# Kernel optimization log

Measured on AMD Instinct MI355X. Metric: run time of the kernel, lower is better.

## Reference

```python
import jax, jax.numpy as jnp
import numpy as np

H = 1024
NH = 16
HD = H // NH
EPS = 1e-5


def setup_inputs() -> dict:
    key = jax.random.key(0)
    ks = jax.random.split(key, 16)
    B, LQ, LK = 2, 1024, 2048
    s = 1.0 / np.sqrt(H)
    inp = {
        "query": jax.random.normal(ks[0], (B, LQ, H), jnp.float32),
        "key": jax.random.normal(ks[1], (B, LK, H), jnp.float32),
        "value": jax.random.normal(ks[2], (B, LK, H), jnp.float32),
        "mask": jax.random.randint(ks[3], (B, LQ, LK), 0, 2, jnp.int32),
        "Wq": jax.random.normal(ks[4], (H, H), jnp.float32) * s,
        "bq": jnp.zeros((H,), jnp.float32),
        "Wk": jax.random.normal(ks[5], (H, H), jnp.float32) * s,
        "bk": jnp.zeros((H,), jnp.float32),
        "Wv": jax.random.normal(ks[6], (H, H), jnp.float32) * s,
        "bv": jnp.zeros((H,), jnp.float32),
        "Wo": jax.random.normal(ks[7], (H, H), jnp.float32) * s,
        "bo": jnp.zeros((H,), jnp.float32),
        "ln_g": jnp.ones((H,), jnp.float32),
        "ln_b": jnp.zeros((H,), jnp.float32),
    }
    return inp


def _split_heads(x, B, L):
    # [B, L, H] -> [B, NH, L, HD]
    return x.reshape(B, L, NH, HD).transpose(0, 2, 1, 3)


def reference(query, key, value, mask, Wq, bq, Wk, bk, Wv, bv, Wo, bo, ln_g, ln_b):
    B, LQ, _ = query.shape
    LK = key.shape[1]
    # projections (torch Linear: x @ W.T + b)
    Q = _split_heads(query @ Wq.T + bq, B, LQ)   # [B,NH,LQ,HD]
    K = _split_heads(key   @ Wk.T + bk, B, LK)   # [B,NH,LK,HD]
    V = _split_heads(value @ Wv.T + bv, B, LK)   # [B,NH,LK,HD]
    scores = jnp.einsum('bhqd,bhkd->bhqk', Q, K) / np.sqrt(HD)
    scores = jnp.where(mask[:, None, :, :] == 0, jnp.float32(-1e9), scores)
    attn = jax.nn.softmax(scores, axis=-1)
    # dropout is identity in eval mode
    ctx = jnp.einsum('bhqk,bhkd->bhqd', attn, V)            # [B,NH,LQ,HD]
    ctx = ctx.transpose(0, 2, 1, 3).reshape(B, LQ, H)       # [B,LQ,H]
    out = ctx @ Wo.T + bo
    x = out + query
    mu = jnp.mean(x, axis=-1, keepdims=True)
    var = jnp.mean(jnp.square(x - mu), axis=-1, keepdims=True)
    return (x - mu) / jnp.sqrt(var + EPS) * ln_g + ln_b
```

## Files before the change

### kernel.cpp

```cpp
#include <hip/hip_runtime.h>
#include <hip/hip_bf16.h>

typedef __hip_bfloat16 hbf16;

#define Hdim 1024
#define NHEAD 16
#define HDIM 64
#define BATCH 2
#define LQ 1024
#define LK 2048
#define LN_EPS 1e-5f

typedef __bf16 bfv8 __attribute__((ext_vector_type(8)));
typedef float floatx4 __attribute__((ext_vector_type(4)));
typedef union { bfv8 v; __bf16 b[8]; unsigned short s[8]; } bfu8;

#define BK 32
#define LDS_PITCH 40
#define QT 64
#define KT 64
#define KS_PITCH 72
#define VT_OFF(d) ((d) * 72 + (((d) >> 3) << 3))
#define PS_OFF(r) ((r) * 72 + (((r) >> 2) << 3))

__device__ inline bfv8 cvt2(const float4 x, const float4 y) {
    bfv8 r = {(__bf16)x.x, (__bf16)x.y, (__bf16)x.z, (__bf16)x.w,
              (__bf16)y.x, (__bf16)y.y, (__bf16)y.z, (__bf16)y.w};
    return r;
}

__global__ __launch_bounds__(256) void proj3_mfma(
    const float* __restrict__ q_in, const float* __restrict__ k_in,
    const float* __restrict__ v_in,
    const float* __restrict__ Wq, const float* __restrict__ bq,
    const float* __restrict__ Wk, const float* __restrict__ bk,
    const float* __restrict__ Wv, const float* __restrict__ bv,
    hbf16* __restrict__ Qp, hbf16* __restrict__ Kp, hbf16* __restrict__ Vp) {
    const int z = blockIdx.z;
    if (z == 0 && blockIdx.y >= (BATCH * LQ) / 64) return;
    const float* A; const float* W; const float* bias; hbf16* out; float scale;
    if (z == 0)      { A = q_in; W = Wq; bias = bq; out = Qp; scale = 0.125f; }
    else if (z == 1) { A = k_in; W = Wk; bias = bk; out = Kp; scale = 1.0f; }
    else             { A = v_in; W = Wv; bias = bv; out = Vp; scale = 1.0f; }

    __shared__ __align__(16) __bf16 As[64 * LDS_PITCH];
    __shared__ __align__(16) __bf16 Bs[64 * LDS_PITCH];
    const int tid = threadIdx.x;
    const int lane = tid & 63;
    const int w = tid >> 6;
    const int wm = w & 1, wn = w >> 1;
    const int rowBase = blockIdx.y * 64;
    const int colBase = blockIdx.x * 64;
    const int sr = tid >> 2;
    const int scg = (tid & 3) * 8;
    const int lr = lane & 15;
    const int quad = lane >> 4;

    floatx4 acc[2][2] = {};

    for (int k0 = 0; k0 < Hdim; k0 += BK) {
        const float* ap = A + (size_t)(rowBase + sr) * Hdim + k0 + scg;
        bfv8 av = cvt2(((const float4*)ap)[0], ((const float4*)ap)[1]);
        const float* wp = W + (size_t)(colBase + sr) * Hdim + k0 + scg;
        bfv8 bv8 = cvt2(((const float4*)wp)[0], ((const float4*)wp)[1]);
        __syncthreads();
        *(bfv8*)&As[sr * LDS_PITCH + scg] = av;
        *(bfv8*)&Bs[sr * LDS_PITCH + scg] = bv8;
        __syncthreads();

        bfv8 bf[2];
#pragma unroll
        for (int nt = 0; nt < 2; ++nt)
            bf[nt] = *(const bfv8*)&Bs[(wn * 32 + nt * 16 + lr) * LDS_PITCH + quad * 8];
#pragma unroll
        for (int mt = 0; mt < 2; ++mt) {
            bfv8 af = *(const bfv8*)&As[(wm * 32 + mt * 16 + lr) * LDS_PITCH + quad * 8];
#pragma unroll
            for (int nt = 0; nt < 2; ++nt)
                acc[mt][nt] = __builtin_amdgcn_mfma_f32_16x16x32_bf16(af, bf[nt], acc[mt][nt], 0, 0, 0);
        }
    }

#pragma unroll
    for (int mt = 0; mt < 2; ++mt)
#pragma unroll
        for (int nt = 0; nt < 2; ++nt) {
            const int n = colBase + wn * 32 + nt * 16 + lr;
            const float bn = bias[n];
#pragma unroll
            for (int rr = 0; rr < 4; ++rr) {
                const int m = rowBase + wm * 32 + mt * 16 + quad * 4 + rr;
                out[(size_t)m * Hdim + n] = __float2bfloat16((acc[mt][nt][rr] + bn) * scale);
            }
        }
}

__global__ __launch_bounds__(256) void gemm_mfma_f32(const float* __restrict__ A,
                                                     const float* __restrict__ W,
                                                     const float* __restrict__ bias,
                                                     hbf16* __restrict__ out,
                                                     float scale) {
    __shared__ __align__(16) __bf16 As[64 * LDS_PITCH];
    __shared__ __align__(16) __bf16 Bs[64 * LDS_PITCH];
    const int tid = threadIdx.x;
    const int lane = tid & 63;
    const int w = tid >> 6;
    const int wm = w & 1, wn = w >> 1;
    const int rowBase = blockIdx.y * 64;
    const int colBase = blockIdx.x * 64;
    const int sr = tid >> 2;
    const int scg = (tid & 3) * 8;
    const int lr = lane & 15;
    const int quad = lane >> 4;

    floatx4 acc[2][2] = {};

    for (int k0 = 0; k0 < Hdim; k0 += BK) {
        const float* ap = A + (size_t)(rowBase + sr) * Hdim + k0 + scg;
        bfv8 av = cvt2(((const float4*)ap)[0], ((const float4*)ap)[1]);
        const float* wp = W + (size_t)(colBase + sr) * Hdim + k0 + scg;
        bfv8 bv = cvt2(((const float4*)wp)[0], ((const float4*)wp)[1]);
        __syncthreads();
        *(bfv8*)&As[sr * LDS_PITCH + scg] = av;
        *(bfv8*)&Bs[sr * LDS_PITCH + scg] = bv;
        __syncthreads();

        bfv8 bf[2];
#pragma unroll
        for (int nt = 0; nt < 2; ++nt)
            bf[nt] = *(const bfv8*)&Bs[(wn * 32 + nt * 16 + lr) * LDS_PITCH + quad * 8];
#pragma unroll
        for (int mt = 0; mt < 2; ++mt) {
            bfv8 af = *(const bfv8*)&As[(wm * 32 + mt * 16 + lr) * LDS_PITCH + quad * 8];
#pragma unroll
            for (int nt = 0; nt < 2; ++nt)
                acc[mt][nt] = __builtin_amdgcn_mfma_f32_16x16x32_bf16(af, bf[nt], acc[mt][nt], 0, 0, 0);
        }
    }

#pragma unroll
    for (int mt = 0; mt < 2; ++mt)
#pragma unroll
        for (int nt = 0; nt < 2; ++nt) {
            const int n = colBase + wn * 32 + nt * 16 + lr;
            const float bn = bias[n];
#pragma unroll
            for (int rr = 0; rr < 4; ++rr) {
                const int m = rowBase + wm * 32 + mt * 16 + quad * 4 + rr;
                out[(size_t)m * Hdim + n] = __float2bfloat16((acc[mt][nt][rr] + bn) * scale);
            }
        }
}

__global__ __launch_bounds__(256) void gemm_mfma_ctx(const hbf16* __restrict__ A,
                                                     const float* __restrict__ W,
                                                     const float* __restrict__ bias,
                                                     const float* __restrict__ resid,
                                                     float* __restrict__ out) {
    __shared__ __align__(16) __bf16 As[64 * LDS_PITCH];
    __shared__ __align__(16) __bf16 Bs[64 * LDS_PITCH];
    const int tid = threadIdx.x;
    const int lane = tid & 63;
    const int w = tid >> 6;
    const int wm = w & 1, wn = w >> 1;
    const int rowBase = blockIdx.y * 64;
    const int colBase = blockIdx.x * 64;
    const int sr = tid >> 2;
    const int scg = (tid & 3) * 8;
    const int lr = lane & 15;
    const int quad = lane >> 4;

    floatx4 acc[2][2] = {};

    for (int k0 = 0; k0 < Hdim; k0 += BK) {
        bfv8 av = *(const bfv8*)(A + (size_t)(rowBase + sr) * Hdim + k0 + scg);
        const float* wp = W + (size_t)(colBase + sr) * Hdim + k0 + scg;
        bfv8 bv = cvt2(((const float4*)wp)[0], ((const float4*)wp)[1]);
        __syncthreads();
        *(bfv8*)&As[sr * LDS_PITCH + scg] = av;
        *(bfv8*)&Bs[sr * LDS_PITCH + scg] = bv;
        __syncthreads();

        bfv8 bf[2];
#pragma unroll
        for (int nt = 0; nt < 2; ++nt)
            bf[nt] = *(const bfv8*)&Bs[(wn * 32 + nt * 16 + lr) * LDS_PITCH + quad * 8];
#pragma unroll
        for (int mt = 0; mt < 2; ++mt) {
            bfv8 af = *(const bfv8*)&As[(wm * 32 + mt * 16 + lr) * LDS_PITCH + quad * 8];
#pragma unroll
            for (int nt = 0; nt < 2; ++nt)
                acc[mt][nt] = __builtin_amdgcn_mfma_f32_16x16x32_bf16(af, bf[nt], acc[mt][nt], 0, 0, 0);
        }
    }

#pragma unroll
    for (int mt = 0; mt < 2; ++mt)
#pragma unroll
        for (int nt = 0; nt < 2; ++nt) {
            const int n = colBase + wn * 32 + nt * 16 + lr;
            const float bn = bias[n];
#pragma unroll
            for (int rr = 0; rr < 4; ++rr) {
                const int m = rowBase + wm * 32 + mt * 16 + quad * 4 + rr;
                out[(size_t)m * Hdim + n] = acc[mt][nt][rr] + bn + resid[(size_t)m * Hdim + n];
            }
        }
}

__global__ __launch_bounds__(256) void mask_prep_st(const int* __restrict__ mask,
                                                    hbf16* __restrict__ mbias) {
    const int t = blockIdx.x;
    const int kt = t & 31;
    const int qb = (t >> 5) & 15;
    const int b = t >> 9;
    const int tid = threadIdx.x;
    const int w = tid >> 6;
    const int lane = tid & 63;
    const int quad = lane >> 4;
    const int u = lane & 15;
    const int qrow = qb * 64 + w * 16 + quad * 4;
    const int kcol = kt * 64 + u;
    const int* mp = mask + ((size_t)(b * LQ + qrow)) * LK + kcol;

    bfu8 v0, v1;
#pragma unroll
    for (int ns = 0; ns < 4; ++ns)
#pragma unroll
        for (int rr = 0; rr < 4; ++rr) {
            const int mv = mp[(size_t)rr * LK + ns * 16];
            const __bf16 bias = (mv == 0) ? (__bf16)(-1e9f) : (__bf16)(-10.0f);
            const int j = ns * 4 + rr;
            if (j < 8) v0.b[j] = bias; else v1.b[j - 8] = bias;
        }
    __bf16* dst = (__bf16*)mbias + (size_t)t * 4096 + tid * 16;
    *(bfv8*)dst = v0.v;
    *(bfv8*)(dst + 8) = v1.v;
}

__global__ __launch_bounds__(256, 4) void attn_split(const hbf16* __restrict__ Qp,
                                                     const hbf16* __restrict__ Kp,
                                                     const hbf16* __restrict__ Vp,
                                                     const hbf16* __restrict__ mbias,
                                                     float* __restrict__ Opart,
                                                     float* __restrict__ lpart) {
    const int qb = blockIdx.x;
    const int h = blockIdx.y;
    const int b = blockIdx.z >> 1;
    const int sp = blockIdx.z & 1;
    const int tid = threadIdx.x;
    const int lane = tid & 63;
    const int w = tid >> 6;
    const int u = lane & 15;
    const int quad = lane >> 4;
    const int qBase = qb * QT;

    __shared__ __align__(16) __bf16 Ks[64 * KS_PITCH];
    __shared__ __align__(16) __bf16 Vt[4672];
    __shared__ __align__(16) __bf16 Ps[4][1184];

    const int qrow_frag = qBase + w * 16 + u;
    const hbf16* qptr = Qp + (size_t)(b * LQ + qrow_frag) * Hdim + h * HDIM + quad * 8;
    const bfv8 af_q0 = *(const bfv8*)qptr;
    const bfv8 af_q1 = *(const bfv8*)(qptr + 32);

    float l_acc[4] = {0.f, 0.f, 0.f, 0.f};
    floatx4 acc_o[4];
#pragma unroll
    for (int nd = 0; nd < 4; ++nd) acc_o[nd] = (floatx4){0.f, 0.f, 0.f, 0.f};

    const int sk = tid >> 2;
    const int sdg = (tid & 3) * 16;
    const int vk2 = (tid >> 3) * 2;
    const int vd0 = (tid & 7) * 8;
    const __bf16* mbT = (const __bf16*)mbias + (size_t)(b * 16 + qb) * 32 * 4096 + tid * 16;

    const int kt0 = sp * (LK / KT / 2);
    for (int kt = kt0; kt < kt0 + (LK / KT / 2); ++kt) {
        const int kBase = kt * KT;

        bfu8 mb0, mb1;
        mb0.v = *(const bfv8*)(mbT + (size_t)kt * 4096);
        mb1.v = *(const bfv8*)(mbT + (size_t)kt * 4096 + 8);

        const hbf16* vp0 = Vp + (size_t)(b * LK + kBase + vk2) * Hdim + h * HDIM + vd0;
        bfu8 v0, v1;
        v0.v = *(const bfv8*)vp0;
        v1.v = *(const bfv8*)(vp0 + Hdim);
        const hbf16* kp = Kp + (size_t)(b * LK + kBase + sk) * Hdim + h * HDIM + sdg;
        const bfv8 kv0 = *(const bfv8*)kp;
        const bfv8 kv1 = *(const bfv8*)(kp + 8);

        __syncthreads();
        *(bfv8*)&Ks[sk * KS_PITCH + sdg] = kv0;
        *(bfv8*)&Ks[sk * KS_PITCH + sdg + 8] = kv1;
#pragma unroll
        for (int i = 0; i < 8; ++i) {
            unsigned int pk = (unsigned int)v0.s[i] | ((unsigned int)v1.s[i] << 16);
            *(unsigned int*)&Vt[VT_OFF(vd0 + i) + vk2] = pk;
        }
        __syncthreads();

        floatx4 acc_s[4];
#pragma unroll
        for (int ns = 0; ns < 4; ++ns) {
            const bfv8 bk0 = *(const bfv8*)&Ks[(ns * 16 + u) * KS_PITCH + quad * 8];
            const bfv8 bk1 = *(const bfv8*)&Ks[(ns * 16 + u) * KS_PITCH + quad * 8 + 32];
            floatx4 a = (floatx4){0.f, 0.f, 0.f, 0.f};
            a = __builtin_amdgcn_mfma_f32_16x16x32_bf16(af_q0, bk0, a, 0, 0, 0);
            a = __builtin_amdgcn_mfma_f32_16x16x32_bf16(af_q1, bk1, a, 0, 0, 0);
            acc_s[ns] = a;
        }

        __bf16* Pw = Ps[w];
#pragma unroll
        for (int ns = 0; ns < 4; ++ns)
#pragma unroll
            for (int rr = 0; rr < 4; ++rr) {
                const int j = ns * 4 + rr;
                const float bias = (j < 8) ? (float)mb0.b[j] : (float)mb1.b[j - 8];
                const float p = __expf(acc_s[ns][rr] + bias);
                Pw[PS_OFF(quad * 4 + rr) + ns * 16 + u] = (__bf16)p;
                l_acc[rr] += p;
            }

        const bfv8 af_p0 = *(const bfv8*)&Pw[PS_OFF(u) + quad * 8];
        const bfv8 af_p1 = *(const bfv8*)&Pw[PS_OFF(u) + quad * 8 + 32];
#pragma unroll
        for (int nd = 0; nd < 4; ++nd) {
            const bfv8 bv0 = *(const bfv8*)&Vt[VT_OFF(nd * 16 + u) + quad * 8];
            const bfv8 bv1 = *(const bfv8*)&Vt[VT_OFF(nd * 16 + u) + quad * 8 + 32];
            acc_o[nd] = __builtin_amdgcn_mfma_f32_16x16x32_bf16(af_p0, bv0, acc_o[nd], 0, 0, 0);
            acc_o[nd] = __builtin_amdgcn_mfma_f32_16x16x32_bf16(af_p1, bv1, acc_o[nd], 0, 0, 0);
        }
    }

#pragma unroll
    for (int rr = 0; rr < 4; ++rr) {
        float l = l_acc[rr];
        l += __shfl_xor(l, 1, 64);
        l += __shfl_xor(l, 2, 64);
        l += __shfl_xor(l, 4, 64);
        l += __shfl_xor(l, 8, 64);
        const int qrow = qBase + w * 16 + quad * 4 + rr;
        const size_t m = (size_t)(b * LQ + qrow);
        float* orow = Opart + (size_t)sp * (BATCH * LQ * Hdim) + m * Hdim + h * HDIM;
#pragma unroll
        for (int nd = 0; nd < 4; ++nd)
            orow[nd * 16 + u] = acc_o[nd][rr];
        if (u == 0)
            lpart[(size_t)sp * (BATCH * LQ * NHEAD) + m * NHEAD + h] = l;
    }
}

__global__ __launch_bounds__(256) void merge_ctx(const float* __restrict__ Opart,
                                                 const float* __restrict__ lpart,
                                                 hbf16* __restrict__ ctx) {
    const size_t m = blockIdx.x;
    const int t = threadIdx.x;
    const int kk = t * 4;
    const int h = kk >> 6;
    const float l = lpart[m * NHEAD + h] +
                    lpart[(size_t)(BATCH * LQ * NHEAD) + m * NHEAD + h];
    const float invl = 1.0f / l;
    const float4 a = ((const float4*)(Opart + m * Hdim))[t];
    const float4 c = ((const float4*)(Opart + (size_t)(BATCH * LQ * Hdim) + m * Hdim))[t];
    hbf16* crow = ctx + m * Hdim + kk;
    crow[0] = __float2bfloat16((a.x + c.x) * invl);
    crow[1] = __float2bfloat16((a.y + c.y) * invl);
    crow[2] = __float2bfloat16((a.z + c.z) * invl);
    crow[3] = __float2bfloat16((a.w + c.w) * invl);
}

__global__ __launch_bounds__(256, 4) void attn_flash_st(const hbf16* __restrict__ Qp,
                                                        const hbf16* __restrict__ Kp,
                                                        const hbf16* __restrict__ Vp,
                                                        const hbf16* __restrict__ mbias,
                                                        hbf16* __restrict__ ctx) {
    const int qb = blockIdx.x;
    const int h = blockIdx.y;
    const int b = blockIdx.z;
    const int tid = threadIdx.x;
    const int lane = tid & 63;
    const int w = tid >> 6;
    const int u = lane & 15;
    const int quad = lane >> 4;
    const int qBase = qb * QT;

    __shared__ __align__(16) __bf16 Ks[64 * KS_PITCH];
    __shared__ __align__(16) __bf16 Vt[4672];
    __shared__ __align__(16) __bf16 Ps[4][1184];

    const int qrow_frag = qBase + w * 16 + u;
    const hbf16* qptr = Qp + (size_t)(b * LQ + qrow_frag) * Hdim + h * HDIM + quad * 8;
    const bfv8 af_q0 = *(const bfv8*)qptr;
    const bfv8 af_q1 = *(const bfv8*)(qptr + 32);

    float l_acc[4] = {0.f, 0.f, 0.f, 0.f};
    floatx4 acc_o[4];
#pragma unroll
    for (int nd = 0; nd < 4; ++nd) acc_o[nd] = (floatx4){0.f, 0.f, 0.f, 0.f};

    const int sk = tid >> 2;
    const int sdg = (tid & 3) * 16;
    const int vk2 = (tid >> 3) * 2;
    const int vd0 = (tid & 7) * 8;
    const __bf16* mbT = (const __bf16*)mbias + (size_t)(b * 16 + qb) * 32 * 4096 + tid * 16;

    for (int kt = 0; kt < LK / KT; ++kt) {
        const int kBase = kt * KT;

        bfu8 mb0, mb1;
        mb0.v = *(const bfv8*)(mbT + (size_t)kt * 4096);
        mb1.v = *(const bfv8*)(mbT + (size_t)kt * 4096 + 8);

        const hbf16* vp0 = Vp + (size_t)(b * LK + kBase + vk2) * Hdim + h * HDIM + vd0;
        bfu8 v0, v1;
        v0.v = *(const bfv8*)vp0;
        v1.v = *(const bfv8*)(vp0 + Hdim);
        const hbf16* kp = Kp + (size_t)(b * LK + kBase + sk) * Hdim + h * HDIM + sdg;
        const bfv8 kv0 = *(const bfv8*)kp;
        const bfv8 kv1 = *(const bfv8*)(kp + 8);

        __syncthreads();
        *(bfv8*)&Ks[sk * KS_PITCH + sdg] = kv0;
        *(bfv8*)&Ks[sk * KS_PITCH + sdg + 8] = kv1;
#pragma unroll
        for (int i = 0; i < 8; ++i) {
            unsigned int pk = (unsigned int)v0.s[i] | ((unsigned int)v1.s[i] << 16);
            *(unsigned int*)&Vt[VT_OFF(vd0 + i) + vk2] = pk;
        }
        __syncthreads();

        floatx4 acc_s[4];
#pragma unroll
        for (int ns = 0; ns < 4; ++ns) {
            const bfv8 bk0 = *(const bfv8*)&Ks[(ns * 16 + u) * KS_PITCH + quad * 8];
            const bfv8 bk1 = *(const bfv8*)&Ks[(ns * 16 + u) * KS_PITCH + quad * 8 + 32];
            floatx4 a = (floatx4){0.f, 0.f, 0.f, 0.f};
            a = __builtin_amdgcn_mfma_f32_16x16x32_bf16(af_q0, bk0, a, 0, 0, 0);
            a = __builtin_amdgcn_mfma_f32_16x16x32_bf16(af_q1, bk1, a, 0, 0, 0);
            acc_s[ns] = a;
        }

        __bf16* Pw = Ps[w];
#pragma unroll
        for (int ns = 0; ns < 4; ++ns)
#pragma unroll
            for (int rr = 0; rr < 4; ++rr) {
                const int j = ns * 4 + rr;
                const float bias = (j < 8) ? (float)mb0.b[j] : (float)mb1.b[j - 8];
                const float p = __expf(acc_s[ns][rr] + bias);
                Pw[PS_OFF(quad * 4 + rr) + ns * 16 + u] = (__bf16)p;
                l_acc[rr] += p;
            }

        const bfv8 af_p0 = *(const bfv8*)&Pw[PS_OFF(u) + quad * 8];
        const bfv8 af_p1 = *(const bfv8*)&Pw[PS_OFF(u) + quad * 8 + 32];
#pragma unroll
        for (int nd = 0; nd < 4; ++nd) {
            const bfv8 bv0 = *(const bfv8*)&Vt[VT_OFF(nd * 16 + u) + quad * 8];
            const bfv8 bv1 = *(const bfv8*)&Vt[VT_OFF(nd * 16 + u) + quad * 8 + 32];
            acc_o[nd] = __builtin_amdgcn_mfma_f32_16x16x32_bf16(af_p0, bv0, acc_o[nd], 0, 0, 0);
            acc_o[nd] = __builtin_amdgcn_mfma_f32_16x16x32_bf16(af_p1, bv1, acc_o[nd], 0, 0, 0);
        }
    }

#pragma unroll
    for (int rr = 0; rr < 4; ++rr) {
        float l = l_acc[rr];
        l += __shfl_xor(l, 1, 64);
        l += __shfl_xor(l, 2, 64);
        l += __shfl_xor(l, 4, 64);
        l += __shfl_xor(l, 8, 64);
        const float invl = 1.0f / l;
        const int qrow = qBase + w * 16 + quad * 4 + rr;
        hbf16* crow = ctx + (size_t)(b * LQ + qrow) * Hdim + h * HDIM;
#pragma unroll
        for (int nd = 0; nd < 4; ++nd)
            crow[nd * 16 + u] = __float2bfloat16(acc_o[nd][rr] * invl);
    }
}

__global__ __launch_bounds__(256) void ln_kernel(float* __restrict__ x,
                                                 const float* __restrict__ g,
                                                 const float* __restrict__ beta) {
    const int row = blockIdx.x;
    float* xr = x + (size_t)row * Hdim;
    __shared__ float red[256];
    const int tid = threadIdx.x;

    const float4 xi = ((const float4*)xr)[tid];
    red[tid] = xi.x + xi.y + xi.z + xi.w;
    __syncthreads();
    for (int st = 128; st > 0; st >>= 1) {
        if (tid < st) red[tid] += red[tid + st];
        __syncthreads();
    }
    const float mu = red[0] * (1.0f / Hdim);
    __syncthreads();
    {
        float dx = xi.x - mu, dy = xi.y - mu, dz = xi.z - mu, dw = xi.w - mu;
        red[tid] = dx * dx + dy * dy + dz * dz + dw * dw;
    }
    __syncthreads();
    for (int st = 128; st > 0; st >>= 1) {
        if (tid < st) red[tid] += red[tid + st];
        __syncthreads();
    }
    const float rstd = rsqrtf(red[0] * (1.0f / Hdim) + LN_EPS);

    const float4 g4 = ((const float4*)g)[tid];
    const float4 b4 = ((const float4*)beta)[tid];
    float4 y;
    y.x = (xi.x - mu) * rstd * g4.x + b4.x;
    y.y = (xi.y - mu) * rstd * g4.y + b4.y;
    y.z = (xi.z - mu) * rstd * g4.z + b4.z;
    y.w = (xi.w - mu) * rstd * g4.w + b4.w;
    ((float4*)xr)[tid] = y;
}

__device__ inline float wave_red_sum(float v) {
    v += __shfl_down(v, 32, 64);
    v += __shfl_down(v, 16, 64);
    v += __shfl_down(v, 8, 64);
    v += __shfl_down(v, 4, 64);
    v += __shfl_down(v, 2, 64);
    v += __shfl_down(v, 1, 64);
    return v;
}

__global__ __launch_bounds__(256) void fused_mha(
    const float* __restrict__ q_in, const float* __restrict__ k_in,
    const float* __restrict__ v_in, const int* __restrict__ mask,
    const float* __restrict__ Wq, const float* __restrict__ bq,
    const float* __restrict__ Wk, const float* __restrict__ bk,
    const float* __restrict__ Wv, const float* __restrict__ bv,
    const float* __restrict__ Wo, const float* __restrict__ bo,
    const float* __restrict__ ln_g, const float* __restrict__ ln_b,
    float* __restrict__ out) {
    const int q = blockIdx.x;
    const int b = blockIdx.y;
    const int tid = threadIdx.x;
    const int lane = tid & 63;
    const int w = tid >> 6;

    __shared__ float qrow[Hdim];
    __shared__ float qt[Hdim];
    __shared__ float sc[LK];
    __shared__ float u[Hdim];
    __shared__ float ctxv[Hdim];
    __shared__ float Qh[HDIM];
    __shared__ float red[256];
    __shared__ float sb_sh;

    const float* qp = q_in + (size_t)(b * LQ + q) * Hdim;
    for (int i = tid; i < Hdim; i += 256) qrow[i] = qp[i];
    __syncthreads();

    const float* keyb = k_in + (size_t)b * LK * Hdim;
    const float* valb = v_in + (size_t)b * LK * Hdim;
    const int* mrow = mask + (size_t)(b * LQ + q) * LK;

    for (int h = 0; h < NHEAD; ++h) {
        for (int dd = w; dd < HDIM; dd += 4) {
            const float4* wrow = (const float4*)(Wq + (size_t)(h * HDIM + dd) * Hdim);
            const float4* q4 = (const float4*)qrow;
            float p = 0.f;
#pragma unroll
            for (int i0 = 0; i0 < 4; ++i0) {
                float4 a = wrow[i0 * 64 + lane];
                float4 c = q4[i0 * 64 + lane];
                p += a.x * c.x + a.y * c.y + a.z * c.z + a.w * c.w;
            }
            p = wave_red_sum(p);
            if (lane == 0) Qh[dd] = p + bq[h * HDIM + dd];
        }
        __syncthreads();

        if (tid < HDIM) red[tid] = Qh[tid] * bk[h * HDIM + tid];

        float4 s4 = {0.f, 0.f, 0.f, 0.f};
        for (int d = 0; d < HDIM; ++d) {
            float4 a = ((const float4*)(Wk + (size_t)(h * HDIM + d) * Hdim))[tid];
            float qd = Qh[d];
            s4.x += a.x * qd;
            s4.y += a.y * qd;
            s4.z += a.z * qd;
            s4.w += a.w * qd;
        }
        __syncthreads();
        if (tid == 0) {
            float s = 0.f;
            for (int i = 0; i < HDIM; ++i) s += red[i];
            sb_sh = s;
        }
        ((float4*)qt)[tid] = s4;
        __syncthreads();
        const float sb = sb_sh;

        for (int k = w; k < LK; k += 4) {
            const float4* krow = (const float4*)(keyb + (size_t)k * Hdim);
            const float4* q4 = (const float4*)qt;
            float p = 0.f;
#pragma unroll
            for (int i0 = 0; i0 < 4; ++i0) {
                float4 a = krow[i0 * 64 + lane];
                float4 c = q4[i0 * 64 + lane];
                p += a.x * c.x + a.y * c.y + a.z * c.z + a.w * c.w;
            }
            p = wave_red_sum(p);
            if (lane == 0) {
                float s = (p + sb) * 0.125f;
                if (mrow[k] == 0) s = -1e9f;
                sc[k] = s;
            }
        }
        __syncthreads();

        float m = -1e30f;
        for (int k = tid; k < LK; k += 256) m = fmaxf(m, sc[k]);
        red[tid] = m;
        __syncthreads();
        for (int s = 128; s > 0; s >>= 1) {
            if (tid < s) red[tid] = fmaxf(red[tid], red[tid + s]);
            __syncthreads();
        }
        const float mx = red[0];
        __syncthreads();
        float sum = 0.f;
        for (int k = tid; k < LK; k += 256) {
            float e = __expf(sc[k] - mx);
            sc[k] = e;
            sum += e;
        }
        red[tid] = sum;
        __syncthreads();
        for (int s = 128; s > 0; s >>= 1) {
            if (tid < s) red[tid] += red[tid + s];
            __syncthreads();
        }
        const float inv = 1.0f / red[0];
        for (int k = tid; k < LK; k += 256) sc[k] *= inv;
        __syncthreads();

        {
            float4 acc = {0.f, 0.f, 0.f, 0.f};
            const float4* vb4 = (const float4*)valb;
#pragma unroll 4
            for (int k = 0; k < LK; ++k) {
                float p = sc[k];
                float4 a = vb4[(size_t)k * (Hdim / 4) + tid];
                acc.x += a.x * p;
                acc.y += a.y * p;
                acc.z += a.z * p;
                acc.w += a.w * p;
            }
            ((float4*)u)[tid] = acc;
        }
        __syncthreads();

        for (int dd = w; dd < HDIM; dd += 4) {
            const float4* wrow = (const float4*)(Wv + (size_t)(h * HDIM + dd) * Hdim);
            const float4* u4 = (const float4*)u;
            float p = 0.f;
#pragma unroll
            for (int i0 = 0; i0 < 4; ++i0) {
                float4 a = wrow[i0 * 64 + lane];
                float4 c = u4[i0 * 64 + lane];
                p += a.x * c.x + a.y * c.y + a.z * c.z + a.w * c.w;
            }
            p = wave_red_sum(p);
            if (lane == 0) ctxv[h * HDIM + dd] = p + bv[h * HDIM + dd];
        }
        __syncthreads();
    }

    for (int n = w; n < Hdim; n += 4) {
        const float4* wrow = (const float4*)(Wo + (size_t)n * Hdim);
        const float4* c4 = (const float4*)ctxv;
        float p = 0.f;
#pragma unroll
        for (int i0 = 0; i0 < 4; ++i0) {
            float4 a = wrow[i0 * 64 + lane];
            float4 c = c4[i0 * 64 + lane];
            p += a.x * c.x + a.y * c.y + a.z * c.z + a.w * c.w;
        }
        p = wave_red_sum(p);
        if (lane == 0) qt[n] = p + bo[n] + qrow[n];
    }
    __syncthreads();

    {
        const float4 x4 = ((const float4*)qt)[tid];
        red[tid] = x4.x + x4.y + x4.z + x4.w;
    }
    __syncthreads();
    for (int s = 128; s > 0; s >>= 1) {
        if (tid < s) red[tid] += red[tid + s];
        __syncthreads();
    }
    const float mu = red[0] * (1.0f / Hdim);
    __syncthreads();
    {
        const float4 x4 = ((const float4*)qt)[tid];
        float dx = x4.x - mu, dy = x4.y - mu, dz = x4.z - mu, dw = x4.w - mu;
        red[tid] = dx * dx + dy * dy + dz * dz + dw * dw;
    }
    __syncthreads();
    for (int s = 128; s > 0; s >>= 1) {
        if (tid < s) red[tid] += red[tid + s];
        __syncthreads();
    }
    const float rstd = rsqrtf(red[0] * (1.0f / Hdim) + LN_EPS);

    float* orow = out + (size_t)(b * LQ + q) * Hdim;
    const float4 x4 = ((const float4*)qt)[tid];
    const float4 g4 = ((const float4*)ln_g)[tid];
    const float4 b4 = ((const float4*)ln_b)[tid];
    float4 y;
    y.x = (x4.x - mu) * rstd * g4.x + b4.x;
    y.y = (x4.y - mu) * rstd * g4.y + b4.y;
    y.z = (x4.z - mu) * rstd * g4.z + b4.z;
    y.w = (x4.w - mu) * rstd * g4.w + b4.w;
    ((float4*)orow)[tid] = y;
}

extern "C" void kernel_launch(void* const* d_in, const int* in_sizes, int n_in,
                              void* d_out, int out_size, void* d_ws, size_t ws_size,
                              hipStream_t stream) {
    const float* query = (const float*)d_in[0];
    const float* key   = (const float*)d_in[1];
    const float* value = (const float*)d_in[2];
    const int*   mask  = (const int*)d_in[3];
    const float* Wq = (const float*)d_in[4];
    const float* bq = (const float*)d_in[5];
    const float* Wk = (const float*)d_in[6];
    const float* bk = (const float*)d_in[7];
    const float* Wv = (const float*)d_in[8];
    const float* bv = (const float*)d_in[9];
    const float* Wo = (const float*)d_in[10];
    const float* bo = (const float*)d_in[11];
    const float* ln_g = (const float*)d_in[12];
    const float* ln_b = (const float*)d_in[13];
    float* out = (float*)d_out;

    const size_t MB = 1024 * 1024;
    dim3 blk(256);

    if (ws_size >= 50 * MB) {
        char* p = (char*)d_ws;
        hbf16* Qp = (hbf16*)p;    p += 4 * MB;
        hbf16* Kp = (hbf16*)p;    p += 8 * MB;
        hbf16* Vp = (hbf16*)p;    p += 8 * MB;
        hbf16* ctxb = (hbf16*)p;  p += 4 * MB;
        hbf16* mbias = (hbf16*)p; p += 8 * MB;
        float* Opart = (float*)p; p += 16 * MB;
        float* lpart = (float*)p; p += 1 * MB;

        proj3_mfma<<<dim3(Hdim / 64, (BATCH * LK) / 64, 3), blk, 0, stream>>>(
            query, key, value, Wq, bq, Wk, bk, Wv, bv, Qp, Kp, Vp);
        mask_prep_st<<<dim3(1024), blk, 0, stream>>>(mask, mbias);

        attn_split<<<dim3(LQ / QT, NHEAD, BATCH * 2), blk, 0, stream>>>(
            Qp, Kp, Vp, mbias, Opart, lpart);
        merge_ctx<<<dim3(BATCH * LQ), blk, 0, stream>>>(Opart, lpart, ctxb);

        gemm_mfma_ctx<<<dim3(Hdim / 64, (BATCH * LQ) / 64), blk, 0, stream>>>(ctxb, Wo, bo, query, out);
        ln_kernel<<<BATCH * LQ, blk, 0, stream>>>(out, ln_g, ln_b);
    } else if (ws_size >= 32 * MB) {
        char* p = (char*)d_ws;
        hbf16* Qp = (hbf16*)p;    p += 4 * MB;
        hbf16* Kp = (hbf16*)p;    p += 8 * MB;
        hbf16* Vp = (hbf16*)p;    p += 8 * MB;
        hbf16* ctxb = (hbf16*)p;  p += 4 * MB;
        hbf16* mbias = (hbf16*)p; p += 8 * MB;

        gemm_mfma_f32<<<dim3(Hdim / 64, (BATCH * LQ) / 64), blk, 0, stream>>>(query, Wq, bq, Qp, 0.125f);
        gemm_mfma_f32<<<dim3(Hdim / 64, (BATCH * LK) / 64), blk, 0, stream>>>(key, Wk, bk, Kp, 1.0f);
        gemm_mfma_f32<<<dim3(Hdim / 64, (BATCH * LK) / 64), blk, 0, stream>>>(value, Wv, bv, Vp, 1.0f);
        mask_prep_st<<<dim3(1024), blk, 0, stream>>>(mask, mbias);
        attn_flash_st<<<dim3(LQ / QT, NHEAD, BATCH), blk, 0, stream>>>(Qp, Kp, Vp, mbias, ctxb);
        gemm_mfma_ctx<<<dim3(Hdim / 64, (BATCH * LQ) / 64), blk, 0, stream>>>(ctxb, Wo, bo, query, out);
        ln_kernel<<<BATCH * LQ, blk, 0, stream>>>(out, ln_g, ln_b);
    } else {
        fused_mha<<<dim3(LQ, BATCH), dim3(256), 0, stream>>>(
            query, key, value, mask, Wq, bq, Wk, bk, Wv, bv, Wo, bo, ln_g, ln_b, out);
    }
}
```

Baseline: 277.6 us.

## Pre-convert inputs to bf16 and use direct-to-LDS loads with 128x128 GEMM tiles

```diff
diff --git a/kernel.cpp b/kernel.cpp
--- a/kernel.cpp
+++ b/kernel.cpp
@@ -27,6 +27,177 @@
     bfv8 r = {(__bf16)x.x, (__bf16)x.y, (__bf16)x.z, (__bf16)x.w,
               (__bf16)y.x, (__bf16)y.y, (__bf16)y.z, (__bf16)y.w};
     return r;
+}
+
+__device__ __forceinline__ void glds16(const void* g, void* l) {
+    __builtin_amdgcn_global_load_lds(
+        (const __attribute__((address_space(1))) void*)g,
+        (__attribute__((address_space(3))) void*)l, 16, 0, 0);
+}
+
+__global__ __launch_bounds__(256) void cvt_all(
+    const float* __restrict__ q, const float* __restrict__ k,
+    const float* __restrict__ v, const float* __restrict__ Wq,
+    const float* __restrict__ Wk, const float* __restrict__ Wv,
+    hbf16* __restrict__ qb, hbf16* __restrict__ kb, hbf16* __restrict__ vb,
+    hbf16* __restrict__ Wqb, hbf16* __restrict__ Wkb, hbf16* __restrict__ Wvb) {
+    const int blk = blockIdx.x;
+    const float* src; hbf16* dst; int base;
+    if (blk < 1024)      { src = q;  dst = qb;  base = blk; }
+    else if (blk < 3072) { src = k;  dst = kb;  base = blk - 1024; }
+    else if (blk < 5120) { src = v;  dst = vb;  base = blk - 3072; }
+    else if (blk < 5632) { src = Wq; dst = Wqb; base = blk - 5120; }
+    else if (blk < 6144) { src = Wk; dst = Wkb; base = blk - 5632; }
+    else                 { src = Wv; dst = Wvb; base = blk - 6144; }
+    const size_t e = (size_t)base * 2048 + (size_t)threadIdx.x * 8;
+    const float4 a = *(const float4*)(src + e);
+    const float4 b = *(const float4*)(src + e + 4);
+    *(bfv8*)((__bf16*)dst + e) = cvt2(a, b);
+}
+
+__global__ __launch_bounds__(256) void proj3_glds(
+    const hbf16* __restrict__ qb, const hbf16* __restrict__ kb,
+    const hbf16* __restrict__ vb,
+    const hbf16* __restrict__ Wqb, const hbf16* __restrict__ Wkb,
+    const hbf16* __restrict__ Wvb,
+    const float* __restrict__ bq, const float* __restrict__ bk,
+    const float* __restrict__ bv,
+    hbf16* __restrict__ Qp, hbf16* __restrict__ Kp, hbf16* __restrict__ Vp) {
+    const int z = blockIdx.z;
+    if (z == 0 && blockIdx.y >= (BATCH * LQ) / 128) return;
+    const hbf16* A; const hbf16* W; const float* bias; hbf16* out; float scale;
+    if (z == 0)      { A = qb; W = Wqb; bias = bq; out = Qp; scale = 0.125f; }
+    else if (z == 1) { A = kb; W = Wkb; bias = bk; out = Kp; scale = 1.0f; }
+    else             { A = vb; W = Wvb; bias = bv; out = Vp; scale = 1.0f; }
+
+    __shared__ __align__(16) __bf16 As[128 * 32];
+    __shared__ __align__(16) __bf16 Bs[128 * 32];
+    const int tid = threadIdx.x;
+    const int lane = tid & 63;
+    const int w = tid >> 6;
+    const int wm = w & 1, wn = w >> 1;
+    const int u = lane & 15;
+    const int quad = lane >> 4;
+    const int rowBase = blockIdx.y * 128;
+    const int colBase = blockIdx.x * 128;
+
+    const int srow = tid >> 2;
+    const int scol = (tid & 3) * 8;
+    const hbf16* aP = A + (size_t)(rowBase + srow) * Hdim + scol;
+    const hbf16* wP = W + (size_t)(colBase + srow) * Hdim + scol;
+    __bf16* ldsA = &As[srow * 32 + scol];
+    __bf16* ldsB = &Bs[srow * 32 + scol];
+
+    floatx4 acc[4][4];
+#pragma unroll
+    for (int mi = 0; mi < 4; ++mi)
+#pragma unroll
+        for (int ni = 0; ni < 4; ++ni) acc[mi][ni] = (floatx4){0.f, 0.f, 0.f, 0.f};
+
+    for (int k0 = 0; k0 < Hdim; k0 += 32) {
+        __syncthreads();
+        glds16(aP + k0, ldsA);
+        glds16(aP + k0 + (size_t)64 * Hdim, ldsA + 64 * 32);
+        glds16(wP + k0, ldsB);
+        glds16(wP + k0 + (size_t)64 * Hdim, ldsB + 64 * 32);
+        __syncthreads();
+
+        bfv8 af[4], bf[4];
+#pragma unroll
+        for (int mi = 0; mi < 4; ++mi)
+            af[mi] = *(const bfv8*)&As[(wm * 64 + mi * 16 + u) * 32 + quad * 8];
+#pragma unroll
+        for (int ni = 0; ni < 4; ++ni)
+            bf[ni] = *(const bfv8*)&Bs[(wn * 64 + ni * 16 + u) * 32 + quad * 8];
+#pragma unroll
+        for (int mi = 0; mi < 4; ++mi)
+#pragma unroll
+            for (int ni = 0; ni < 4; ++ni)
+                acc[mi][ni] = __builtin_amdgcn_mfma_f32_16x16x32_bf16(af[mi], bf[ni], acc[mi][ni], 0, 0, 0);
+    }
+
+#pragma unroll
+    for (int mi = 0; mi < 4; ++mi)
+#pragma unroll
+        for (int ni = 0; ni < 4; ++ni) {
+            const int n = colBase + wn * 64 + ni * 16 + u;
+            const float bn = bias[n];
+#pragma unroll
+            for (int rr = 0; rr < 4; ++rr) {
+                const int m = rowBase + wm * 64 + mi * 16 + quad * 4 + rr;
+                out[(size_t)m * Hdim + n] = __float2bfloat16((acc[mi][ni][rr] + bn) * scale);
+            }
+        }
+}
+
+__global__ __launch_bounds__(256) void gemm_ctx_glds(const hbf16* __restrict__ A,
+                                                     const float* __restrict__ W,
+                                                     const float* __restrict__ bias,
+                                                     const float* __restrict__ resid,
+                                                     float* __restrict__ out) {
+    __shared__ __align__(16) __bf16 As[128 * 32];
+    __shared__ __align__(16) __bf16 Bs[128 * 32];
+    const int tid = threadIdx.x;
+    const int lane = tid & 63;
+    const int w = tid >> 6;
+    const int wm = w & 1, wn = w >> 1;
+    const int u = lane & 15;
+    const int quad = lane >> 4;
+    const int rowBase = blockIdx.y * 128;
+    const int colBase = blockIdx.x * 128;
+
+    const int srow = tid >> 2;
+    const int scol = (tid & 3) * 8;
+    const hbf16* aP = A + (size_t)(rowBase + srow) * Hdim + scol;
+    __bf16* ldsA = &As[srow * 32 + scol];
+
+    const int brow = tid >> 1;
+    const int bcol = (tid & 1) * 16;
+    const float* wP = W + (size_t)(colBase + brow) * Hdim + bcol;
+    __bf16* ldsBw = &Bs[brow * 32 + bcol];
+
+    floatx4 acc[4][4];
+#pragma unroll
+    for (int mi = 0; mi < 4; ++mi)
+#pragma unroll
+        for (int ni = 0; ni < 4; ++ni) acc[mi][ni] = (floatx4){0.f, 0.f, 0.f, 0.f};
+
+    for (int k0 = 0; k0 < Hdim; k0 += 32) {
+        const float4* w4 = (const float4*)(wP + k0);
+        const float4 w0 = w4[0], w1 = w4[1], w2 = w4[2], w3 = w4[3];
+        __syncthreads();
+        glds16(aP + k0, ldsA);
+        glds16(aP + k0 + (size_t)64 * Hdim, ldsA + 64 * 32);
+        *(bfv8*)ldsBw = cvt2(w0, w1);
+        *(bfv8*)(ldsBw + 8) = cvt2(w2, w3);
+        __syncthreads();
+
+        bfv8 af[4], bf[4];
+#pragma unroll
+        for (int mi = 0; mi < 4; ++mi)
+            af[mi] = *(const bfv8*)&As[(wm * 64 + mi * 16 + u) * 32 + quad * 8];
+#pragma unroll
+        for (int ni = 0; ni < 4; ++ni)
+            bf[ni] = *(const bfv8*)&Bs[(wn * 64 + ni * 16 + u) * 32 + quad * 8];
+#pragma unroll
+        for (int mi = 0; mi < 4; ++mi)
+#pragma unroll
+            for (int ni = 0; ni < 4; ++ni)
+                acc[mi][ni] = __builtin_amdgcn_mfma_f32_16x16x32_bf16(af[mi], bf[ni], acc[mi][ni], 0, 0, 0);
+    }
+
+#pragma unroll
+    for (int mi = 0; mi < 4; ++mi)
+#pragma unroll
+        for (int ni = 0; ni < 4; ++ni) {
+            const int n = colBase + wn * 64 + ni * 16 + u;
+            const float bn = bias[n];
+#pragma unroll
+            for (int rr = 0; rr < 4; ++rr) {
+                const int m = rowBase + wm * 64 + mi * 16 + quad * 4 + rr;
+                out[(size_t)m * Hdim + n] = acc[mi][ni][rr] + bn + resid[(size_t)m * Hdim + n];
+            }
+        }
 }
 
 __global__ __launch_bounds__(256) void proj3_mfma(
@@ -750,23 +921,33 @@
 
     if (ws_size >= 50 * MB) {
         char* p = (char*)d_ws;
-        hbf16* Qp = (hbf16*)p;    p += 4 * MB;
-        hbf16* Kp = (hbf16*)p;    p += 8 * MB;
-        hbf16* Vp = (hbf16*)p;    p += 8 * MB;
-        hbf16* ctxb = (hbf16*)p;  p += 4 * MB;
-        hbf16* mbias = (hbf16*)p; p += 8 * MB;
-        float* Opart = (float*)p; p += 16 * MB;
-        float* lpart = (float*)p; p += 1 * MB;
-
-        proj3_mfma<<<dim3(Hdim / 64, (BATCH * LK) / 64, 3), blk, 0, stream>>>(
-            query, key, value, Wq, bq, Wk, bk, Wv, bv, Qp, Kp, Vp);
+        hbf16* Qp    = (hbf16*)(p + 0 * MB);
+        hbf16* Kp    = (hbf16*)(p + 4 * MB);
+        hbf16* Vp    = (hbf16*)(p + 12 * MB);
+        hbf16* ctxb  = (hbf16*)(p + 20 * MB);
+        hbf16* mbias = (hbf16*)(p + 24 * MB);
+        float* Opart = (float*)(p + 32 * MB);
+        float* lpart = (float*)(p + 48 * MB);
+
+        hbf16* qb  = (hbf16*)(p + 20 * MB);
+        hbf16* kb  = (hbf16*)(p + 24 * MB);
+        hbf16* vb  = (hbf16*)(p + 32 * MB);
+        hbf16* Wqb = (hbf16*)(p + 40 * MB);
+        hbf16* Wkb = (hbf16*)(p + 42 * MB);
+        hbf16* Wvb = (hbf16*)(p + 44 * MB);
+
+        cvt_all<<<dim3(6656), blk, 0, stream>>>(query, key, value, Wq, Wk, Wv,
+                                                qb, kb, vb, Wqb, Wkb, Wvb);
+        proj3_glds<<<dim3(Hdim / 128, (BATCH * LK) / 128, 3), blk, 0, stream>>>(
+            qb, kb, vb, Wqb, Wkb, Wvb, bq, bk, bv, Qp, Kp, Vp);
         mask_prep_st<<<dim3(1024), blk, 0, stream>>>(mask, mbias);
 
         attn_split<<<dim3(LQ / QT, NHEAD, BATCH * 2), blk, 0, stream>>>(
             Qp, Kp, Vp, mbias, Opart, lpart);
         merge_ctx<<<dim3(BATCH * LQ), blk, 0, stream>>>(Opart, lpart, ctxb);
 
-        gemm_mfma_ctx<<<dim3(Hdim / 64, (BATCH * LQ) / 64), blk, 0, stream>>>(ctxb, Wo, bo, query, out);
+        gemm_ctx_glds<<<dim3(Hdim / 128, (BATCH * LQ) / 128), blk, 0, stream>>>(
+            ctxb, Wo, bo, query, out);
         ln_kernel<<<BATCH * LQ, blk, 0, stream>>>(out, ln_g, ln_b);
     } else if (ws_size >= 32 * MB) {
         char* p = (char*)d_ws;
```

Result: faster. 261.5 us (-5.8%).
